# Kernel optimization log

Measured on AMD Instinct MI355X. Metric: run time of the kernel, lower is better.

The kernel has to match this reference:

```python
import jax, jax.numpy as jnp
import numpy as np

TOP_K = 2  # matches init_kwargs top_k


def setup_inputs() -> dict:
    key = jax.random.key(0)
    ks = jax.random.split(key, 5)
    B, T, C, H, E = 4, 1024, 768, 3072, 8
    x = jax.random.normal(ks[0], (B, T, C), dtype=jnp.float32)
    Wg = jax.random.normal(ks[1], (C, E), dtype=jnp.float32) * 0.02
    W1 = jax.random.normal(ks[2], (E, C, H), dtype=jnp.float32) * (1.0 / np.sqrt(C))
    b1 = jnp.zeros((E, H), dtype=jnp.float32)
    W2 = jax.random.normal(ks[3], (E, H, C), dtype=jnp.float32) * (1.0 / np.sqrt(H))
    b2 = jnp.zeros((E, C), dtype=jnp.float32)
    return {"x": x, "Wg": Wg, "W1": W1, "b1": b1, "W2": W2, "b2": b2}


def reference(x, Wg, W1, b1, W2, b2):
    # TopKRouter: softmax over expert logits, keep top-k probs, zeros elsewhere.
    E = Wg.shape[-1]
    logits = jnp.einsum('btc,ce->bte', x, Wg)
    probs = jax.nn.softmax(logits, axis=-1)
    top_vals, top_idx = jax.lax.top_k(probs, TOP_K)          # (B,T,K)
    gates = (jax.nn.one_hot(top_idx, E, dtype=probs.dtype) * top_vals[..., None]).sum(-2)  # (B,T,E)

    # Per-expert FFN (Linear -> ReLU -> Linear; dropout is identity in eval),
    # combined with sparse gate weights (only top-k entries are nonzero).
    h = jax.nn.relu(jnp.einsum('btc,ech->bteh', x, W1) + b1)  # (B,T,E,H)
    y = jnp.einsum('bteh,ehc->btec', h, W2) + b2              # (B,T,E,C)
    out = jnp.einsum('bte,btec->btc', gates, y)               # (B,T,C)
    return out
```

## Files before the change

kernel.cpp:

```cpp
#include <hip/hip_runtime.h>
#include <hip/hip_bf16.h>
#include <cmath>

#define NT    4096
#define CDIM  768
#define HDIM  3072
#define NEXP  8
#define CAP   1280

typedef __bf16 bf16_t;
typedef __bf16 bf16x8 __attribute__((ext_vector_type(8)));
typedef float  f32x4  __attribute__((ext_vector_type(4)));

__device__ __forceinline__ void glds16(const void* g, void* l) {
    __builtin_amdgcn_global_load_lds(
        (const __attribute__((address_space(1))) void*)g,
        (__attribute__((address_space(3))) void*)l, 16, 0, 0);
}

template<int R, int CC>
__global__ __launch_bounds__(256)
void transpose_convert_kernel(const float* __restrict__ in, bf16_t* __restrict__ out) {
    __shared__ float tile[64][68];
    int e = blockIdx.z;
    int c0 = blockIdx.x * 64, r0 = blockIdx.y * 64;
    const float* src = in + (size_t)e * R * CC;
    bf16_t* dst = out + (size_t)e * R * CC;
    int t = threadIdx.x;
    int c4 = (t & 15) * 4, rr = t >> 4;
    #pragma unroll
    for (int i = 0; i < 4; i++) {
        int r = rr + i * 16;
        float4 v = *reinterpret_cast<const float4*>(&src[(size_t)(r0 + r) * CC + c0 + c4]);
        tile[r][c4 + 0] = v.x; tile[r][c4 + 1] = v.y;
        tile[r][c4 + 2] = v.z; tile[r][c4 + 3] = v.w;
    }
    __syncthreads();
    #pragma unroll
    for (int i = 0; i < 4; i++) {
        int cc = rr + i * 16;
        int r4 = (t & 15) * 4;
        union { bf16_t h[4]; uint2 u; } un;
        un.h[0] = (bf16_t)tile[r4 + 0][cc]; un.h[1] = (bf16_t)tile[r4 + 1][cc];
        un.h[2] = (bf16_t)tile[r4 + 2][cc]; un.h[3] = (bf16_t)tile[r4 + 3][cc];
        *reinterpret_cast<uint2*>(&dst[(size_t)(c0 + cc) * R + r0 + r4]) = un.u;
    }
}

__global__ __launch_bounds__(512)
void router_kernel(const float* __restrict__ x, const float* __restrict__ wg,
                   bf16_t* __restrict__ xb,
                   int* __restrict__ counts, int* __restrict__ tmap,
                   float* __restrict__ gmap, int* __restrict__ smap) {
    __shared__ int lcnt[NEXP];
    __shared__ int gbase[NEXP];
    int tid = threadIdx.x, lane = tid & 63, wid = tid >> 6;
    if (tid < NEXP) lcnt[tid] = 0;
    __syncthreads();

    int ti0[4], ti1[4], tr0[4], tr1[4];
    float tg0[4], tg1[4];

    #pragma unroll
    for (int k = 0; k < 4; k++) {
        int t = blockIdx.x * 32 + wid * 4 + k;
        const float* xr = x + (size_t)t * CDIM;
        float acc[NEXP];
        #pragma unroll
        for (int e = 0; e < NEXP; e++) acc[e] = 0.f;
        #pragma unroll
        for (int i = 0; i < CDIM / 256; i++) {
            int c = (i * 64 + lane) * 4;
            float4 v = *reinterpret_cast<const float4*>(xr + c);
            union { bf16_t h[4]; uint2 u; } un;
            un.h[0] = (bf16_t)v.x; un.h[1] = (bf16_t)v.y;
            un.h[2] = (bf16_t)v.z; un.h[3] = (bf16_t)v.w;
            *reinterpret_cast<uint2*>(xb + (size_t)t * CDIM + c) = un.u;
            float vv[4] = {v.x, v.y, v.z, v.w};
            #pragma unroll
            for (int j = 0; j < 4; j++)
                #pragma unroll
                for (int e = 0; e < NEXP; e++)
                    acc[e] += vv[j] * wg[(c + j) * NEXP + e];
        }
        #pragma unroll
        for (int e = 0; e < NEXP; e++) {
            #pragma unroll
            for (int off = 32; off > 0; off >>= 1)
                acc[e] += __shfl_xor(acc[e], off, 64);
        }
        if (lane == 0) {
            float mx = acc[0];
            #pragma unroll
            for (int e = 1; e < NEXP; e++) mx = fmaxf(mx, acc[e]);
            float p[NEXP], s = 0.f;
            #pragma unroll
            for (int e = 0; e < NEXP; e++) { p[e] = expf(acc[e] - mx); s += p[e]; }
            float inv = 1.f / s;
            int i0 = 0;
            #pragma unroll
            for (int e = 1; e < NEXP; e++) if (p[e] > p[i0]) i0 = e;
            int i1 = (i0 == 0) ? 1 : 0;
            #pragma unroll
            for (int e = 0; e < NEXP; e++) if (e != i0 && p[e] > p[i1]) i1 = e;
            ti0[k] = i0; ti1[k] = i1;
            tg0[k] = p[i0] * inv; tg1[k] = p[i1] * inv;
            tr0[k] = atomicAdd(&lcnt[i0], 1);
            tr1[k] = atomicAdd(&lcnt[i1], 1);
        }
    }
    __syncthreads();
    if (tid < NEXP) gbase[tid] = atomicAdd(&counts[tid], lcnt[tid]);
    __syncthreads();
    if (lane == 0) {
        #pragma unroll
        for (int k = 0; k < 4; k++) {
            int t = blockIdx.x * 32 + wid * 4 + k;
            int c0 = gbase[ti0[k]] + tr0[k]; if (c0 >= CAP) c0 = CAP - 1;
            int c1 = gbase[ti1[k]] + tr1[k]; if (c1 >= CAP) c1 = CAP - 1;
            int s0 = ti0[k] * CAP + c0, s1 = ti1[k] * CAP + c1;
            tmap[s0] = t; gmap[s0] = tg0[k]; smap[t * 2]     = s0;
            tmap[s1] = t; gmap[s1] = tg1[k]; smap[t * 2 + 1] = s1;
        }
    }
}

__global__ __launch_bounds__(256)
void moe_gemm1_kernel(const bf16_t* __restrict__ xb, const bf16_t* __restrict__ w1t,
                      const float* __restrict__ b1, const int* __restrict__ counts,
                      const int* __restrict__ tmap, bf16_t* __restrict__ hws) {
    int h = blockIdx.x;
    int e = h & 7;
    int local = h >> 3;
    int mt = local / (HDIM / 128);
    int nt = local - mt * (HDIM / 128);
    int cnt = counts[e]; if (cnt > CAP) cnt = CAP;
    if (mt * 128 >= cnt) return;
    int m0 = e * CAP + mt * 128;
    int rend = e * CAP + cnt;
    int n0 = nt * 128;

    __shared__ __attribute__((aligned(16))) bf16_t As[128 * 32];
    __shared__ __attribute__((aligned(16))) bf16_t Bs[128 * 32];

    int tid = threadIdx.x, lane = tid & 63, wid = tid >> 6;
    const bf16_t* aP[2];
    const bf16_t* bP[2];
    int reg[2];
    #pragma unroll
    for (int it = 0; it < 2; it++) {
        int region = wid * 2 + it;
        int row = region * 16 + (lane >> 2);
        int kk = (lane & 3) * 8;
        int pos = m0 + row;
        if (pos > rend - 1) pos = rend - 1;
        aP[it] = xb + (size_t)tmap[pos] * CDIM + kk;
        bP[it] = w1t + ((size_t)e * HDIM + n0 + row) * CDIM + kk;
        reg[it] = region * 512;
    }

    int wm = (wid >> 1) * 64, wn = (wid & 1) * 64;
    int q = lane >> 4, mr = lane & 15;

    f32x4 acc[4][4];
    #pragma unroll
    for (int i = 0; i < 4; i++)
        #pragma unroll
        for (int j = 0; j < 4; j++)
            acc[i][j] = (f32x4){0.f, 0.f, 0.f, 0.f};

    for (int k0 = 0; k0 < CDIM; k0 += 32) {
        #pragma unroll
        for (int it = 0; it < 2; it++) {
            glds16(aP[it] + k0, As + reg[it]);
            glds16(bP[it] + k0, Bs + reg[it]);
        }
        __syncthreads();
        bf16x8 af[4], bfr[4];
        #pragma unroll
        for (int ti = 0; ti < 4; ti++)
            af[ti] = *reinterpret_cast<const bf16x8*>(&As[(wm + ti * 16 + mr) * 32 + q * 8]);
        #pragma unroll
        for (int tj = 0; tj < 4; tj++)
            bfr[tj] = *reinterpret_cast<const bf16x8*>(&Bs[(wn + tj * 16 + mr) * 32 + q * 8]);
        #pragma unroll
        for (int ti = 0; ti < 4; ti++)
            #pragma unroll
            for (int tj = 0; tj < 4; tj++)
                acc[ti][tj] = __builtin_amdgcn_mfma_f32_16x16x32_bf16(af[ti], bfr[tj], acc[ti][tj], 0, 0, 0);
        __syncthreads();
    }

    const float* be = b1 + (size_t)e * HDIM + n0;
    #pragma unroll
    for (int ti = 0; ti < 4; ti++) {
        #pragma unroll
        for (int r = 0; r < 4; r++) {
            int pos = m0 + wm + ti * 16 + q * 4 + r;
            if (pos < rend) {
                bf16_t* hrow = hws + (size_t)pos * HDIM + n0;
                #pragma unroll
                for (int tj = 0; tj < 4; tj++) {
                    float v = acc[ti][tj][r] + be[wn + tj * 16 + mr];
                    hrow[wn + tj * 16 + mr] = (bf16_t)fmaxf(v, 0.f);
                }
            }
        }
    }
}

__global__ __launch_bounds__(256)
void moe_gemm2_kernel(const bf16_t* __restrict__ hws, const bf16_t* __restrict__ w2t,
                      const float* __restrict__ b2, const int* __restrict__ counts,
                      const float* __restrict__ gmap, float* __restrict__ yws) {
    int h = blockIdx.x;
    int e = h & 7;
    int local = h >> 3;
    int mt = local / (CDIM / 128);
    int nt = local - mt * (CDIM / 128);
    int cnt = counts[e]; if (cnt > CAP) cnt = CAP;
    if (mt * 128 >= cnt) return;
    int m0 = e * CAP + mt * 128;
    int rend = e * CAP + cnt;
    int n0 = nt * 128;

    __shared__ __attribute__((aligned(16))) bf16_t As[128 * 32];
    __shared__ __attribute__((aligned(16))) bf16_t Bs[128 * 32];

    int tid = threadIdx.x, lane = tid & 63, wid = tid >> 6;
    const bf16_t* aP[2];
    const bf16_t* bP[2];
    int reg[2];
    #pragma unroll
    for (int it = 0; it < 2; it++) {
        int region = wid * 2 + it;
        int row = region * 16 + (lane >> 2);
        int kk = (lane & 3) * 8;
        int pos = m0 + row;
        if (pos > rend - 1) pos = rend - 1;
        aP[it] = hws + (size_t)pos * HDIM + kk;
        bP[it] = w2t + ((size_t)e * CDIM + n0 + row) * HDIM + kk;
        reg[it] = region * 512;
    }

    int wm = (wid >> 1) * 64, wn = (wid & 1) * 64;
    int q = lane >> 4, mr = lane & 15;

    f32x4 acc[4][4];
    #pragma unroll
    for (int i = 0; i < 4; i++)
        #pragma unroll
        for (int j = 0; j < 4; j++)
            acc[i][j] = (f32x4){0.f, 0.f, 0.f, 0.f};

    for (int k0 = 0; k0 < HDIM; k0 += 32) {
        #pragma unroll
        for (int it = 0; it < 2; it++) {
            glds16(aP[it] + k0, As + reg[it]);
            glds16(bP[it] + k0, Bs + reg[it]);
        }
        __syncthreads();
        bf16x8 af[4], bfr[4];
        #pragma unroll
        for (int ti = 0; ti < 4; ti++)
            af[ti] = *reinterpret_cast<const bf16x8*>(&As[(wm + ti * 16 + mr) * 32 + q * 8]);
        #pragma unroll
        for (int tj = 0; tj < 4; tj++)
            bfr[tj] = *reinterpret_cast<const bf16x8*>(&Bs[(wn + tj * 16 + mr) * 32 + q * 8]);
        #pragma unroll
        for (int ti = 0; ti < 4; ti++)
            #pragma unroll
            for (int tj = 0; tj < 4; tj++)
                acc[ti][tj] = __builtin_amdgcn_mfma_f32_16x16x32_bf16(af[ti], bfr[tj], acc[ti][tj], 0, 0, 0);
        __syncthreads();
    }

    const float* be = b2 + (size_t)e * CDIM + n0;
    #pragma unroll
    for (int ti = 0; ti < 4; ti++) {
        #pragma unroll
        for (int r = 0; r < 4; r++) {
            int pos = m0 + wm + ti * 16 + q * 4 + r;
            if (pos < rend) {
                float g = gmap[pos];
                float* yrow = yws + (size_t)pos * CDIM + n0;
                #pragma unroll
                for (int tj = 0; tj < 4; tj++) {
                    float v = acc[ti][tj][r] + be[wn + tj * 16 + mr];
                    yrow[wn + tj * 16 + mr] = g * v;
                }
            }
        }
    }
}

__global__ __launch_bounds__(256)
void combine_kernel(const float* __restrict__ yws, const int* __restrict__ smap,
                    float* __restrict__ out) {
    int idx = blockIdx.x * 256 + threadIdx.x;
    int t = idx / (CDIM / 4);
    int c = (idx - t * (CDIM / 4)) * 4;
    int s0 = smap[t * 2], s1 = smap[t * 2 + 1];
    float4 a = *reinterpret_cast<const float4*>(yws + (size_t)s0 * CDIM + c);
    float4 b = *reinterpret_cast<const float4*>(yws + (size_t)s1 * CDIM + c);
    float4 o = {a.x + b.x, a.y + b.y, a.z + b.z, a.w + b.w};
    *reinterpret_cast<float4*>(out + (size_t)t * CDIM + c) = o;
}

extern "C" void kernel_launch(void* const* d_in, const int* in_sizes, int n_in,
                              void* d_out, int out_size, void* d_ws, size_t ws_size,
                              hipStream_t stream) {
    const float* x  = (const float*)d_in[0];
    const float* wg = (const float*)d_in[1];
    const float* w1 = (const float*)d_in[2];
    const float* b1 = (const float*)d_in[3];
    const float* w2 = (const float*)d_in[4];
    const float* b2 = (const float*)d_in[5];
    float* out = (float*)d_out;

    char* w = (char*)d_ws;
    size_t off = 0;
    bf16_t* xb  = (bf16_t*)(w + off); off += (size_t)NT * CDIM * 2;
    bf16_t* w1t = (bf16_t*)(w + off); off += (size_t)NEXP * CDIM * HDIM * 2;
    bf16_t* w2t = (bf16_t*)(w + off); off += (size_t)NEXP * CDIM * HDIM * 2;
    bf16_t* hws = (bf16_t*)(w + off); off += (size_t)NEXP * CAP * HDIM * 2;
    float* yws  = (float*)w1t;
    int* counts = (int*)(w + off);  off += 64;
    int* tmap   = (int*)(w + off);  off += (size_t)NEXP * CAP * 4;
    int* smap   = (int*)(w + off);  off += (size_t)NT * 2 * 4;
    float* gmap = (float*)(w + off);

    hipMemsetAsync(counts, 0, NEXP * sizeof(int), stream);

    transpose_convert_kernel<CDIM, HDIM>
        <<<dim3(HDIM / 64, CDIM / 64, NEXP), 256, 0, stream>>>(w1, w1t);
    transpose_convert_kernel<HDIM, CDIM>
        <<<dim3(CDIM / 64, HDIM / 64, NEXP), 256, 0, stream>>>(w2, w2t);
    router_kernel<<<NT / 32, 512, 0, stream>>>(x, wg, xb, counts, tmap, gmap, smap);

    moe_gemm1_kernel<<<8 * (CAP / 128) * (HDIM / 128), 256, 0, stream>>>(
        xb, w1t, b1, counts, tmap, hws);
    moe_gemm2_kernel<<<8 * (CAP / 128) * (CDIM / 128), 256, 0, stream>>>(
        hws, w2t, b2, counts, gmap, yws);
    combine_kernel<<<NT * (CDIM / 4) / 256, 256, 0, stream>>>(yws, smap, out);
}
```

Before: 362.7 us.

## Merge weight transpose kernels and widen bf16 stores; shrink router blocks

Folds the two weight transpose-convert launches into a single prep kernel that picks W1 or W2 from blockIdx.z. Shared-memory tile writes become float4 stores, and global writes are packed as 16-byte groups of 8 bf16 values instead of 8-byte groups. The router now uses 256-thread blocks covering 16 tokens each, so twice as many blocks are launched. This cuts launch overhead and improves store efficiency in the weight conversion, but the 8-row column reads from the shared tile may cause more bank conflicts.

Result: no change. 357.8 us (-1.3%).

```diff
diff --git a/kernel.cpp b/kernel.cpp
--- a/kernel.cpp
+++ b/kernel.cpp
@@ -18,36 +18,41 @@
         (__attribute__((address_space(3))) void*)l, 16, 0, 0);
 }
 
-template<int R, int CC>
-__global__ __launch_bounds__(256)
-void transpose_convert_kernel(const float* __restrict__ in, bf16_t* __restrict__ out) {
+__global__ __launch_bounds__(256)
+void prep_kernel(const float* __restrict__ w1, const float* __restrict__ w2,
+                 bf16_t* __restrict__ w1t, bf16_t* __restrict__ w2t) {
     __shared__ float tile[64][68];
-    int e = blockIdx.z;
-    int c0 = blockIdx.x * 64, r0 = blockIdx.y * 64;
-    const float* src = in + (size_t)e * R * CC;
-    bf16_t* dst = out + (size_t)e * R * CC;
+    int z = blockIdx.z;
+    bool isW1 = z < 8;
+    int e = isW1 ? z : z - 8;
+    int R  = isW1 ? CDIM : HDIM;
+    int CC = isW1 ? HDIM : CDIM;
+    const float* src = (isW1 ? w1 : w2) + (size_t)e * CDIM * HDIM;
+    bf16_t* dst = (isW1 ? w1t : w2t) + (size_t)e * CDIM * HDIM;
+    int ntc = CC / 64;
+    int bx = blockIdx.x;
+    int c0 = (bx % ntc) * 64, r0 = (bx / ntc) * 64;
     int t = threadIdx.x;
     int c4 = (t & 15) * 4, rr = t >> 4;
     #pragma unroll
     for (int i = 0; i < 4; i++) {
         int r = rr + i * 16;
         float4 v = *reinterpret_cast<const float4*>(&src[(size_t)(r0 + r) * CC + c0 + c4]);
-        tile[r][c4 + 0] = v.x; tile[r][c4 + 1] = v.y;
-        tile[r][c4 + 2] = v.z; tile[r][c4 + 3] = v.w;
+        *reinterpret_cast<float4*>(&tile[r][c4]) = v;
     }
     __syncthreads();
-    #pragma unroll
-    for (int i = 0; i < 4; i++) {
-        int cc = rr + i * 16;
-        int r4 = (t & 15) * 4;
-        union { bf16_t h[4]; uint2 u; } un;
-        un.h[0] = (bf16_t)tile[r4 + 0][cc]; un.h[1] = (bf16_t)tile[r4 + 1][cc];
-        un.h[2] = (bf16_t)tile[r4 + 2][cc]; un.h[3] = (bf16_t)tile[r4 + 3][cc];
-        *reinterpret_cast<uint2*>(&dst[(size_t)(c0 + cc) * R + r0 + r4]) = un.u;
-    }
-}
-
-__global__ __launch_bounds__(512)
+    int r8 = (t & 7) * 8;
+    #pragma unroll
+    for (int i = 0; i < 2; i++) {
+        int cc = (t >> 3) + i * 32;
+        union { bf16_t h[8]; uint4 u; } pk;
+        #pragma unroll
+        for (int s = 0; s < 8; s++) pk.h[s] = (bf16_t)tile[r8 + s][cc];
+        *reinterpret_cast<uint4*>(&dst[(size_t)(c0 + cc) * R + r0 + r8]) = pk.u;
+    }
+}
+
+__global__ __launch_bounds__(256)
 void router_kernel(const float* __restrict__ x, const float* __restrict__ wg,
                    bf16_t* __restrict__ xb,
                    int* __restrict__ counts, int* __restrict__ tmap,
@@ -63,7 +68,7 @@
 
     #pragma unroll
     for (int k = 0; k < 4; k++) {
-        int t = blockIdx.x * 32 + wid * 4 + k;
+        int t = blockIdx.x * 16 + wid * 4 + k;
         const float* xr = x + (size_t)t * CDIM;
         float acc[NEXP];
         #pragma unroll
@@ -115,7 +120,7 @@
     if (lane == 0) {
         #pragma unroll
         for (int k = 0; k < 4; k++) {
-            int t = blockIdx.x * 32 + wid * 4 + k;
+            int t = blockIdx.x * 16 + wid * 4 + k;
             int c0 = gbase[ti0[k]] + tr0[k]; if (c0 >= CAP) c0 = CAP - 1;
             int c1 = gbase[ti1[k]] + tr1[k]; if (c1 >= CAP) c1 = CAP - 1;
             int s0 = ti0[k] * CAP + c0, s1 = ti1[k] * CAP + c1;
@@ -332,11 +337,9 @@
 
     hipMemsetAsync(counts, 0, NEXP * sizeof(int), stream);
 
-    transpose_convert_kernel<CDIM, HDIM>
-        <<<dim3(HDIM / 64, CDIM / 64, NEXP), 256, 0, stream>>>(w1, w1t);
-    transpose_convert_kernel<HDIM, CDIM>
-        <<<dim3(CDIM / 64, HDIM / 64, NEXP), 256, 0, stream>>>(w2, w2t);
-    router_kernel<<<NT / 32, 512, 0, stream>>>(x, wg, xb, counts, tmap, gmap, smap);
+    router_kernel<<<NT / 16, 256, 0, stream>>>(x, wg, xb, counts, tmap, gmap, smap);
+    prep_kernel<<<dim3((CDIM / 64) * (HDIM / 64), 1, 16), 256, 0, stream>>>(
+        w1, w2, w1t, w2t);
 
     moe_gemm1_kernel<<<8 * (CAP / 128) * (HDIM / 128), 256, 0, stream>>>(
         xb, w1t, b1, counts, tmap, hws);
```
